# Performance work log

Hardware: AMD Instinct MI355X
Metric: run time of the kernel (lower is better)

Reference implementation:

```python
import jax, jax.numpy as jnp
import numpy as np

B, S, D = 2, 2048, 1024
NH, HD = 16, 64
MLP = 4096
EPS = 1e-6  # flax nnx.RMSNorm default epsilon


def rms_norm(x, scale):
    var = jnp.mean(jnp.square(x.astype(jnp.float32)), axis=-1, keepdims=True)
    return (x * jax.lax.rsqrt(var + EPS)).astype(x.dtype) * scale


def setup_inputs() -> dict:
    key = jax.random.key(0)
    ks = jax.random.split(key, 16)
    lin = lambda k, fin, fout: jax.random.normal(k, (fin, fout), jnp.float32) / np.sqrt(fin)
    x = jax.random.normal(ks[0], (B, S, D), jnp.float32)
    # causal mask [b, s, s]
    mask = jnp.broadcast_to(jnp.tril(jnp.ones((S, S), jnp.bool_))[None], (B, S, S))
    return {
        "x": x,
        "mask": mask,
        "attn_norm_scale": jnp.ones((D,), jnp.float32),
        "q_w": lin(ks[1], D, D), "q_b": jnp.zeros((D,), jnp.float32),
        "k_w": lin(ks[2], D, D), "k_b": jnp.zeros((D,), jnp.float32),
        "v_w": lin(ks[3], D, D), "v_b": jnp.zeros((D,), jnp.float32),
        "o_w": lin(ks[4], D, D), "o_b": jnp.zeros((D,), jnp.float32),
        "ffn_norm_scale": jnp.ones((D,), jnp.float32),
        "gate_w": lin(ks[5], D, MLP), "gate_b": jnp.zeros((MLP,), jnp.float32),
        "up_w": lin(ks[6], D, MLP), "up_b": jnp.zeros((MLP,), jnp.float32),
        "down_w": lin(ks[7], MLP, D), "down_b": jnp.zeros((D,), jnp.float32),
    }


def reference(x, mask, attn_norm_scale, q_w, q_b, k_w, k_b, v_w, v_b, o_w, o_b,
              ffn_norm_scale, gate_w, gate_b, up_w, up_b, down_w, down_b):
    b, s, d = x.shape
    h = rms_norm(x, attn_norm_scale)
    q = (h @ q_w + q_b).reshape(b, s, NH, HD)
    k = (h @ k_w + k_b).reshape(b, s, NH, HD)
    v = (h @ v_w + v_b).reshape(b, s, NH, HD)
    scale = jnp.float32(HD) ** -0.5
    logits = jnp.einsum('bsnh,btnh->bnst', q, k) * scale  # [b, n, s, s]
    logits = jnp.where(mask[:, None, :, :], logits, jnp.finfo(logits.dtype).min)
    attn = jax.nn.softmax(logits.astype(jnp.float32), axis=-1).astype(x.dtype)
    attn_out = jnp.einsum('bnst,btnh->bsnh', attn, v).reshape(b, s, d)
    x = x + attn_out @ o_w + o_b
    h = rms_norm(x, ffn_norm_scale)
    ffn = (jax.nn.silu(h @ gate_w + gate_b) * (h @ up_w + up_b)) @ down_w + down_b
    return x + ffn
```

## Files before the change

kernel.cpp:

```cpp
#include <hip/hip_runtime.h>

#define S_LEN 2048
#define DMODEL 1024
#define NHEADS 16
#define MLPDIM 4096

typedef float f32x4 __attribute__((ext_vector_type(4)));
typedef __bf16 bf16x8 __attribute__((ext_vector_type(8)));
typedef __bf16 bf16x4 __attribute__((ext_vector_type(4)));

__device__ __forceinline__ void gload_lds16(const void* gsrc, void* ldst) {
  __builtin_amdgcn_global_load_lds(
      (const __attribute__((address_space(1))) void*)gsrc,
      (__attribute__((address_space(3))) void*)ldst, 16, 0, 0);
}

#define BARR() __builtin_amdgcn_s_barrier()
#define VMC(n) do { asm volatile("s_waitcnt vmcnt(" #n ")" ::: "memory"); __builtin_amdgcn_sched_barrier(0); } while (0)

__global__ __launch_bounds__(256) void prep_k(
    const float* __restrict__ qw, const float* __restrict__ kw,
    const float* __restrict__ vw, const float* __restrict__ ow,
    const float* __restrict__ gw, const float* __restrict__ uw,
    const float* __restrict__ dw, __bf16* __restrict__ wqkv,
    __bf16* __restrict__ wo, __bf16* __restrict__ wg, __bf16* __restrict__ wu,
    __bf16* __restrict__ wd, const float* __restrict__ qb,
    const float* __restrict__ kb, const float* __restrict__ vb,
    float* __restrict__ bqkv, const float* __restrict__ x,
    const float* __restrict__ ascale, __bf16* __restrict__ hbuf) {
  __shared__ __bf16 tile[64][66];
  __shared__ float part[4];
  int bid = blockIdx.x, t = threadIdx.x;
  if (bid >= 8192) {
    int i = (bid - 8192) * 256 + t;
    if (i < 1024) bqkv[i] = qb[i];
    else if (i < 2048) bqkv[i] = kb[i - 1024];
    else if (i < 3072) bqkv[i] = vb[i - 2048];
    return;
  }
  if (bid >= 4096) {
    int row = bid - 4096;
    f32x4 v = ((const f32x4*)(x + (size_t)row * DMODEL))[t];
    float ss = v[0] * v[0] + v[1] * v[1] + v[2] * v[2] + v[3] * v[3];
#pragma unroll
    for (int off = 1; off < 64; off <<= 1) ss += __shfl_xor(ss, off, 64);
    if ((t & 63) == 0) part[t >> 6] = ss;
    __syncthreads();
    float tot = part[0] + part[1] + part[2] + part[3];
    float r = rsqrtf(tot * (1.0f / DMODEL) + 1e-6f);
    f32x4 s4 = ((const f32x4*)ascale)[t];
    bf16x4 o;
#pragma unroll
    for (int e = 0; e < 4; ++e) o[e] = (__bf16)(v[e] * r * s4[e]);
    ((bf16x4*)hbuf)[(size_t)row * (DMODEL / 4) + t] = o;
    return;
  }
  const float* in;
  __bf16* out;
  int K, N, bx, by;
  if (bid < 1024) {
    int job = bid >> 8, tt = bid & 255;
    K = 1024; N = 1024; bx = tt & 15; by = tt >> 4;
    in = (job == 0) ? qw : (job == 1) ? kw : (job == 2) ? vw : ow;
    out = (job == 0) ? wqkv : (job == 1) ? wqkv + 1024 * 1024
        : (job == 2) ? wqkv + 2 * 1024 * 1024 : wo;
  } else if (bid < 3072) {
    int job = (bid - 1024) >> 10, tt = (bid - 1024) & 1023;
    K = 1024; N = 4096; bx = tt & 63; by = tt >> 6;
    in = job ? uw : gw;
    out = job ? wu : wg;
  } else {
    int tt = bid - 3072;
    K = 4096; N = 1024; bx = tt & 15; by = tt >> 4;
    in = dw; out = wd;
  }
  int n0 = bx * 64, k0 = by * 64;
  int rr = (t & 63) >> 4, sl = t & 15, wv = t >> 6;
#pragma unroll
  for (int j = 0; j < 4; ++j) {
    int r = wv * 4 + rr + j * 16;
    f32x4 v = *(const f32x4*)(in + (size_t)(k0 + r) * N + n0 + sl * 4);
#pragma unroll
    for (int e = 0; e < 4; ++e) tile[r][sl * 4 + e] = (__bf16)v[e];
  }
  __syncthreads();
#pragma unroll
  for (int j = 0; j < 2; ++j) {
    int u = t + j * 256;
    int n = u >> 3, kc = u & 7;
    bf16x8 o;
#pragma unroll
    for (int e = 0; e < 8; ++e) o[e] = tile[kc * 8 + e][n];
    *(bf16x8*)(out + (size_t)(n0 + n) * K + k0 + kc * 8) = o;
  }
}

__global__ __launch_bounds__(256) void rmsnorm_k(
    const float* __restrict__ x, const float* __restrict__ scale,
    __bf16* __restrict__ out) {
  int row = blockIdx.x, tid = threadIdx.x;
  f32x4 v = ((const f32x4*)(x + (size_t)row * DMODEL))[tid];
  float ss = v[0] * v[0] + v[1] * v[1] + v[2] * v[2] + v[3] * v[3];
#pragma unroll
  for (int off = 1; off < 64; off <<= 1) ss += __shfl_xor(ss, off, 64);
  __shared__ float part[4];
  if ((tid & 63) == 0) part[tid >> 6] = ss;
  __syncthreads();
  float tot = part[0] + part[1] + part[2] + part[3];
  float r = rsqrtf(tot * (1.0f / DMODEL) + 1e-6f);
  f32x4 s4 = ((const f32x4*)scale)[tid];
  bf16x4 o;
#pragma unroll
  for (int e = 0; e < 4; ++e) o[e] = (__bf16)(v[e] * r * s4[e]);
  ((bf16x4*)out)[(size_t)row * (DMODEL / 4) + tid] = o;
}

__global__ __launch_bounds__(256, 3) void gemm_qkv(
    const __bf16* __restrict__ A, const __bf16* __restrict__ Bt,
    const float* __restrict__ bias, __bf16* __restrict__ C,
    __bf16* __restrict__ vt, int M, int N, int K) {
  __shared__ __attribute__((aligned(16))) __bf16 As[128 * 64];
  __shared__ __attribute__((aligned(16))) __bf16 Bs[128 * 64];
  int tid = threadIdx.x, lane = tid & 63, wave = tid >> 6;
  int l15 = lane & 15, g4 = lane >> 4;
  int NB = N >> 7, P = M >> 10;
  int xcd = blockIdx.x & 7, j = blockIdx.x >> 3;
  int grp = j / (2 * NB), jj = j - grp * 2 * NB;
  int bm = (xcd * P + grp * 2 + (jj & 1)) * 128;
  int bn = (jj >> 1) * 128;
  int wr = wave >> 1, wc = wave & 1;
  f32x4 acc[4][4] = {};
  const __bf16* Abase = A + (size_t)bm * K;
  const __bf16* Bbase = Bt + (size_t)bn * K;

  for (int k0 = 0; k0 < K; k0 += 64) {
#pragma unroll
    for (int i = 0; i < 4; ++i) {
      int u = tid + i * 256;
      int r = u >> 3, c = (u & 7) ^ (r & 7);
      gload_lds16(Abase + (size_t)r * K + k0 + c * 8, As + u * 8);
      gload_lds16(Bbase + (size_t)r * K + k0 + c * 8, Bs + u * 8);
    }
    __syncthreads();
#pragma unroll
    for (int ks = 0; ks < 2; ++ks) {
      bf16x8 af[4], bfr[4];
#pragma unroll
      for (int m = 0; m < 4; ++m) {
        int r = wr * 64 + m * 16 + l15;
        af[m] = *(const bf16x8*)(As + r * 64 + (((4 * ks + g4) ^ (r & 7)) << 3));
      }
#pragma unroll
      for (int n = 0; n < 4; ++n) {
        int r = wc * 64 + n * 16 + l15;
        bfr[n] = *(const bf16x8*)(Bs + r * 64 + (((4 * ks + g4) ^ (r & 7)) << 3));
      }
      __builtin_amdgcn_s_setprio(1);
#pragma unroll
      for (int m = 0; m < 4; ++m)
#pragma unroll
        for (int n = 0; n < 4; ++n)
          acc[m][n] = __builtin_amdgcn_mfma_f32_16x16x32_bf16(af[m], bfr[n], acc[m][n], 0, 0, 0);
      __builtin_amdgcn_s_setprio(0);
    }
    __syncthreads();
  }
  int r0 = bm + wr * 64 + g4 * 4;
  int c0 = bn + wc * 64 + l15;
  bool isV = (bn >= 2048);
#pragma unroll
  for (int n = 0; n < 4; ++n) {
    int c = c0 + n * 16;
    float bv = bias[c];
#pragma unroll
    for (int m = 0; m < 4; ++m) {
      int rb = r0 + m * 16;
      if (!isV) {
#pragma unroll
        for (int rg = 0; rg < 4; ++rg)
          C[(size_t)(rb + rg) * N + c] = (__bf16)(acc[m][n][rg] + bv);
      } else {
        bf16x4 vv;
#pragma unroll
        for (int rg = 0; rg < 4; ++rg) vv[rg] = (__bf16)(acc[m][n][rg] + bv);
        int b = rb >> 11, s = rb & 2047;
        int sp = (s & ~31) | (((s >> 2) & 3) << 3) | (((s >> 4) & 1) << 2);
        *(bf16x4*)(vt + (size_t)(b * 1024 + c - 2048) * S_LEN + sp) = vv;
      }
    }
  }
}

__global__ __launch_bounds__(256, 4) void gemm_gu(
    const __bf16* __restrict__ A, const __bf16* __restrict__ Gt,
    const __bf16* __restrict__ Ut, const float* __restrict__ gb,
    const float* __restrict__ ub, __bf16* __restrict__ Cout,
    int M, int N, int K) {
  __shared__ __attribute__((aligned(16))) __bf16 As[128 * 64];
  __shared__ __attribute__((aligned(16))) __bf16 Gs[64 * 64];
  __shared__ __attribute__((aligned(16))) __bf16 Us[64 * 64];
  int tid = threadIdx.x, lane = tid & 63, wave = tid >> 6;
  int l15 = lane & 15, g4 = lane >> 4;
  int lin = blockIdx.x;
  int xcd = lin & 7, idx = lin >> 3;
  int bxl = idx >> 4, byl = idx & 15;
  int bn = ((xcd & 3) * 16 + bxl) * 64;
  int bm = ((xcd >> 2) * 16 + byl) * 128;
  int wr = wave >> 1, wc = wave & 1;
  f32x4 ag[4][2] = {}, au[4][2] = {};
  const __bf16* Abase = A + (size_t)bm * K;
  const __bf16* Gbase = Gt + (size_t)bn * K;
  const __bf16* Ubase = Ut + (size_t)bn * K;

  for (int k0 = 0; k0 < K; k0 += 64) {
#pragma unroll
    for (int j = 0; j < 4; ++j) {
      int u = tid + j * 256;
      int r = u >> 3, c = (u & 7) ^ (r & 7);
      gload_lds16(Abase + (size_t)r * K + k0 + c * 8, As + u * 8);
    }
#pragma unroll
    for (int j = 0; j < 2; ++j) {
      int u = tid + j * 256;
      int r = u >> 3, c = (u & 7) ^ (r & 7);
      gload_lds16(Gbase + (size_t)r * K + k0 + c * 8, Gs + u * 8);
      gload_lds16(Ubase + (size_t)r * K + k0 + c * 8, Us + u * 8);
    }
    __syncthreads();
#pragma unroll
    for (int ks = 0; ks < 2; ++ks) {
      bf16x8 af[4], gf[2], uf[2];
#pragma unroll
      for (int m = 0; m < 4; ++m) {
        int r = wr * 64 + m * 16 + l15;
        af[m] = *(const bf16x8*)(As + r * 64 + (((4 * ks + g4) ^ (r & 7)) << 3));
      }
#pragma unroll
      for (int n = 0; n < 2; ++n) {
        int r = wc * 32 + n * 16 + l15;
        int off = r * 64 + (((4 * ks + g4) ^ (r & 7)) << 3);
        gf[n] = *(const bf16x8*)(Gs + off);
        uf[n] = *(const bf16x8*)(Us + off);
      }
      __builtin_amdgcn_s_setprio(1);
#pragma unroll
      for (int m = 0; m < 4; ++m)
#pragma unroll
        for (int n = 0; n < 2; ++n) {
          ag[m][n] = __builtin_amdgcn_mfma_f32_16x16x32_bf16(af[m], gf[n], ag[m][n], 0, 0, 0);
          au[m][n] = __builtin_amdgcn_mfma_f32_16x16x32_bf16(af[m], uf[n], au[m][n], 0, 0, 0);
        }
      __builtin_amdgcn_s_setprio(0);
    }
    __syncthreads();
  }
  int r0 = bm + wr * 64 + g4 * 4;
  int c0 = bn + wc * 32 + l15;
#pragma unroll
  for (int n = 0; n < 2; ++n) {
    int c = c0 + n * 16;
    float gbv = gb[c], ubv = ub[c];
#pragma unroll
    for (int m = 0; m < 4; ++m) {
      int rb = r0 + m * 16;
#pragma unroll
      for (int rg = 0; rg < 4; ++rg) {
        float g = ag[m][n][rg] + gbv;
        float u = au[m][n][rg] + ubv;
        float v = g / (1.0f + __expf(-g)) * u;
        Cout[(size_t)(rb + rg) * N + c] = (__bf16)v;
      }
    }
  }
}

template <int OUT_BF16, int RESID, int SILU>
__global__ __launch_bounds__(256, 3) void gemm_n64(
    const __bf16* __restrict__ A, const __bf16* __restrict__ Bt,
    const float* __restrict__ bias, const float* __restrict__ resid,
    const __bf16* __restrict__ aux, void* __restrict__ Cout,
    int M, int N, int K) {
  __shared__ __attribute__((aligned(16))) __bf16 As[2][128 * 64];
  __shared__ __attribute__((aligned(16))) __bf16 Bs[2][64 * 64];
  int tid = threadIdx.x, lane = tid & 63, wave = tid >> 6;
  int l15 = lane & 15, g4 = lane >> 4;
  int NB = N >> 6;
  int xcd = blockIdx.x & 7, j = blockIdx.x >> 3;
  int grp = j / (2 * NB), jj = j - grp * 2 * NB;
  int bm = (xcd * (M >> 10) + grp * 2 + (jj & 1)) * 128;
  int bn = (jj >> 1) * 64;
  int wr = wave >> 1, wc = wave & 1;
  f32x4 acc[4][2] = {};
  const __bf16* Abase = A + (size_t)bm * K;
  const __bf16* Bbase = Bt + (size_t)bn * K;

  auto stage = [&](int k0, int sb) {
#pragma unroll
    for (int i = 0; i < 4; ++i) {
      int u = tid + i * 256;
      int r = u >> 3, c = (u & 7) ^ (r & 7);
      gload_lds16(Abase + (size_t)r * K + k0 + c * 8, As[sb] + u * 8);
    }
#pragma unroll
    for (int i = 0; i < 2; ++i) {
      int u = tid + i * 256;
      int r = u >> 3, c = (u & 7) ^ (r & 7);
      gload_lds16(Bbase + (size_t)r * K + k0 + c * 8, Bs[sb] + u * 8);
    }
  };

  int NT = K >> 6;
  stage(0, 0);
  for (int t = 0; t < NT; ++t) {
    int sb = t & 1;
    if (t + 1 < NT) { stage((t + 1) << 6, sb ^ 1); VMC(6); }
    else { VMC(0); }
    BARR();
#pragma unroll
    for (int ks = 0; ks < 2; ++ks) {
      bf16x8 af[4], bfr[2];
#pragma unroll
      for (int m = 0; m < 4; ++m) {
        int r = wr * 64 + m * 16 + l15;
        af[m] = *(const bf16x8*)(As[sb] + r * 64 + (((4 * ks + g4) ^ (r & 7)) << 3));
      }
#pragma unroll
      for (int n = 0; n < 2; ++n) {
        int r = wc * 32 + n * 16 + l15;
        bfr[n] = *(const bf16x8*)(Bs[sb] + r * 64 + (((4 * ks + g4) ^ (r & 7)) << 3));
      }
      __builtin_amdgcn_s_setprio(1);
#pragma unroll
      for (int m = 0; m < 4; ++m)
#pragma unroll
        for (int n = 0; n < 2; ++n)
          acc[m][n] = __builtin_amdgcn_mfma_f32_16x16x32_bf16(af[m], bfr[n], acc[m][n], 0, 0, 0);
      __builtin_amdgcn_s_setprio(0);
    }
    BARR();
  }
  int r0 = bm + wr * 64 + g4 * 4;
  int c0 = bn + wc * 32 + l15;
#pragma unroll
  for (int n = 0; n < 2; ++n) {
    int c = c0 + n * 16;
    float bv = bias[c];
#pragma unroll
    for (int m = 0; m < 4; ++m) {
      int rb = r0 + m * 16;
#pragma unroll
      for (int rg = 0; rg < 4; ++rg) {
        int r = rb + rg;
        size_t idx = (size_t)r * N + c;
        float v = acc[m][n][rg] + bv;
        if (SILU) {
          float gg = (float)aux[idx];
          v *= gg / (1.0f + __expf(-gg));
        }
        if (RESID) v += resid[idx];
        if (OUT_BF16) ((__bf16*)Cout)[idx] = (__bf16)v;
        else ((float*)Cout)[idx] = v;
      }
    }
  }
}

#define SCL2E 0.180336879f
__global__ __launch_bounds__(512, 4) void attn_k(
    const __bf16* __restrict__ qkv, const __bf16* __restrict__ vt,
    __bf16* __restrict__ ao) {
  __shared__ __attribute__((aligned(16))) __bf16 Ks[2][128 * 64];
  __shared__ __attribute__((aligned(16))) __bf16 Vs[2][64 * 128];
  int tid = threadIdx.x, lane = tid & 63, w = tid >> 6;
  int l15 = lane & 15, g4 = lane >> 4;
  int bh = blockIdx.x, b = bh >> 4, h = bh & 15;
  int qt = 15 - blockIdx.y;
  int qb = qt * 128;
  int qw = qb + w * 16;
  const __bf16* qkvb = qkv + (size_t)b * S_LEN * 3072 + h * 64;
  const __bf16* kgb = qkvb + 1024;
  const __bf16* vtb = vt + (size_t)b * 1024 * S_LEN + (size_t)(h * 64) * S_LEN;

  bf16x8 qf[2];
#pragma unroll
  for (int ks = 0; ks < 2; ++ks)
    qf[ks] = *(const bf16x8*)(qkvb + (size_t)(qw + l15) * 3072 + 32 * ks + 8 * g4);

  f32x4 oa[4] = {};
  float mrow = -1e30f, lrow = 0.f;
  int q = qw + l15;
  int nt = qt + 1;

  auto stage = [&](int kvb, int buf) {
#pragma unroll
    for (int i = 0; i < 2; ++i) {
      int u = tid + i * 512;
      int r = u >> 3, c = u & 7;
      gload_lds16(kgb + (size_t)(kvb + r) * 3072 + ((c ^ (r & 7)) << 3),
                  Ks[buf] + w * 512 + i * 4096);
    }
#pragma unroll
    for (int i = 0; i < 2; ++i) {
      int u = tid + i * 512;
      int r = u >> 4, cu = u & 15;
      gload_lds16(vtb + (size_t)r * S_LEN + kvb + ((cu ^ (r & 7)) << 3),
                  Vs[buf] + w * 512 + i * 4096);
    }
  };

  stage(0, 0);
  __syncthreads();
  int buf = 0;
  for (int t = 0; t < nt; ++t) {
    int kvb = t * 128;
    if (t + 1 < nt) stage(kvb + 128, buf ^ 1);

    f32x4 sa[8];
#pragma unroll
    for (int i = 0; i < 8; ++i) sa[i] = f32x4{0.f, 0.f, 0.f, 0.f};
#pragma unroll
    for (int st = 0; st < 2; ++st)
#pragma unroll
      for (int ks = 0; ks < 2; ++ks) {
        bf16x8 kf[4];
#pragma unroll
        for (int n = 0; n < 4; ++n) {
          int rr = st * 64 + n * 16 + l15;
          int bc = (64 * ks + 16 * g4) ^ ((rr & 7) << 4);
          kf[n] = *(const bf16x8*)((const char*)Ks[buf] + rr * 128 + bc);
        }
        __builtin_amdgcn_s_setprio(1);
#pragma unroll
        for (int n = 0; n < 4; ++n)
          sa[st * 4 + n] = __builtin_amdgcn_mfma_f32_16x16x32_bf16(kf[n], qf[ks], sa[st * 4 + n], 0, 0, 0);
        __builtin_amdgcn_s_setprio(0);
      }

    bool lastt = (t == nt - 1);
    float nmx = -1e30f;
#pragma unroll
    for (int i = 0; i < 8; ++i)
#pragma unroll
      for (int rg = 0; rg < 4; ++rg) {
        float s = sa[i][rg] * SCL2E;
        if (lastt) {
          int key = kvb + (i >> 2) * 64 + (i & 3) * 16 + 4 * g4 + rg;
          s = (key <= q) ? s : -1e30f;
        }
        sa[i][rg] = s;
        nmx = fmaxf(nmx, s);
      }
    nmx = fmaxf(nmx, __shfl_xor(nmx, 16));
    nmx = fmaxf(nmx, __shfl_xor(nmx, 32));
    float nm;
    if (!__all(nmx <= mrow)) {
      nm = fmaxf(mrow, nmx);
      float sc = exp2f(mrow - nm);
      mrow = nm;
      lrow *= sc;
#pragma unroll
      for (int rg = 0; rg < 4; ++rg) {
        float scq = __shfl(sc, 4 * g4 + rg);
#pragma unroll
        for (int dn = 0; dn < 4; ++dn) oa[dn][rg] *= scq;
      }
    } else {
      nm = mrow;
    }
    float rs = 0.f;
    bf16x8 pa[2][2];
#pragma unroll
    for (int st = 0; st < 2; ++st)
#pragma unroll
      for (int ks = 0; ks < 2; ++ks)
#pragma unroll
        for (int hf = 0; hf < 2; ++hf)
#pragma unroll
          for (int rg = 0; rg < 4; ++rg) {
            float p = exp2f(sa[st * 4 + 2 * ks + hf][rg] - nm);
            rs += p;
            pa[st][ks][hf * 4 + rg] = (__bf16)p;
          }
    rs += __shfl_xor(rs, 16);
    rs += __shfl_xor(rs, 32);
    lrow += rs;

#pragma unroll
    for (int st = 0; st < 2; ++st)
#pragma unroll
      for (int ks = 0; ks < 2; ++ks) {
        __builtin_amdgcn_s_setprio(1);
#pragma unroll
        for (int dn = 0; dn < 4; ++dn) {
          int rr = dn * 16 + l15;
          int swz = (rr & 7) << 4;
          const char* vrow = (const char*)Vs[buf] + rr * 256;
          bf16x8 vf = *(const bf16x8*)(vrow + ((st * 128 + ks * 64 + g4 * 16) ^ swz));
          oa[dn] = __builtin_amdgcn_mfma_f32_16x16x32_bf16(pa[st][ks], vf, oa[dn], 0, 0, 0);
        }
        __builtin_amdgcn_s_setprio(0);
      }
    __syncthreads();
    buf ^= 1;
  }

  __bf16* aobase = ao + (size_t)b * S_LEN * DMODEL + h * 64;
#pragma unroll
  for (int rg = 0; rg < 4; ++rg) {
    float rl = 1.0f / __shfl(lrow, 4 * g4 + rg);
    int qo = qw + 4 * g4 + rg;
#pragma unroll
    for (int dn = 0; dn < 4; ++dn)
      aobase[(size_t)qo * DMODEL + dn * 16 + l15] = (__bf16)(oa[dn][rg] * rl);
  }
}

#define OFF_WQKV 0
#define OFF_WO 6291456
#define OFF_WG 8388608
#define OFF_WU 16777216
#define OFF_WD 25165824
#define OFF_BQKV 33554432
#define OFF_H 33570816
#define OFF_QKV 41959424
#define OFF_AO 67125248
#define OFF_T 75513856
#define OFF_VT OFF_T
#define OFF_X2 109068288

extern "C" void kernel_launch(void* const* d_in, const int* in_sizes, int n_in,
                              void* d_out, int out_size, void* d_ws, size_t ws_size,
                              hipStream_t stream) {
  (void)in_sizes; (void)n_in; (void)out_size; (void)ws_size;
  const float* x = (const float*)d_in[0];
  const float* attn_scale = (const float*)d_in[2];
  const float* q_w = (const float*)d_in[3];
  const float* q_b = (const float*)d_in[4];
  const float* k_w = (const float*)d_in[5];
  const float* k_b = (const float*)d_in[6];
  const float* v_w = (const float*)d_in[7];
  const float* v_b = (const float*)d_in[8];
  const float* o_w = (const float*)d_in[9];
  const float* o_b = (const float*)d_in[10];
  const float* ffn_scale = (const float*)d_in[11];
  const float* gate_w = (const float*)d_in[12];
  const float* gate_b = (const float*)d_in[13];
  const float* up_w = (const float*)d_in[14];
  const float* up_b = (const float*)d_in[15];
  const float* down_w = (const float*)d_in[16];
  const float* down_b = (const float*)d_in[17];

  char* ws = (char*)d_ws;
  __bf16* wqkv = (__bf16*)(ws + OFF_WQKV);
  __bf16* wo = (__bf16*)(ws + OFF_WO);
  __bf16* wg = (__bf16*)(ws + OFF_WG);
  __bf16* wu = (__bf16*)(ws + OFF_WU);
  __bf16* wd = (__bf16*)(ws + OFF_WD);
  float* bqkv = (float*)(ws + OFF_BQKV);
  __bf16* hbuf = (__bf16*)(ws + OFF_H);
  __bf16* qkvbuf = (__bf16*)(ws + OFF_QKV);
  __bf16* aobuf = (__bf16*)(ws + OFF_AO);
  __bf16* tbuf = (__bf16*)(ws + OFF_T);
  __bf16* vtbuf = (__bf16*)(ws + OFF_VT);
  float* x2 = (float*)(ws + OFF_X2);

  dim3 blk(256);
  prep_k<<<dim3(8204), blk, 0, stream>>>(q_w, k_w, v_w, o_w, gate_w, up_w, down_w,
                                         wqkv, wo, wg, wu, wd, q_b, k_b, v_b, bqkv,
                                         x, attn_scale, hbuf);
  gemm_qkv<<<dim3(768), blk, 0, stream>>>(hbuf, wqkv, bqkv, qkvbuf, vtbuf, 4096, 3072, 1024);
  attn_k<<<dim3(32, 16), dim3(512), 0, stream>>>(qkvbuf, vtbuf, aobuf);
  gemm_n64<0, 1, 0><<<dim3(512), blk, 0, stream>>>(aobuf, wo, o_b, x, nullptr, x2, 4096, 1024, 1024);
  rmsnorm_k<<<4096, blk, 0, stream>>>(x2, ffn_scale, hbuf);
  gemm_gu<<<dim3(2048), blk, 0, stream>>>(hbuf, wg, wu, gate_b, up_b, tbuf, 4096, 4096, 1024);
  gemm_n64<0, 1, 0><<<dim3(512), blk, 0, stream>>>(tbuf, wd, down_b, x2, nullptr, (float*)d_out, 4096, 1024, 4096);
}
```

Before: 240.8 us.

## Process two 16-row query groups per wave in attention, halving block threads

The attention kernel now runs 4 waves of 256 threads instead of 8 waves of 512, and each wave handles 32 query rows as two 16-row groups. Each K and V fragment read from LDS feeds two MFMAs, which halves LDS read traffic per MFMA. Staging loops double their iterations to fill the same 128-row K/V tiles. The cost is double the accumulator and score registers per wave and less wave-level parallelism per block to hide latency; launch bounds move to (256, 2).

```diff
diff --git a/kernel.cpp b/kernel.cpp
--- a/kernel.cpp
+++ b/kernel.cpp
@@ -366,7 +366,7 @@
 }
 
 #define SCL2E 0.180336879f
-__global__ __launch_bounds__(512, 4) void attn_k(
+__global__ __launch_bounds__(256, 2) void attn_k(
     const __bf16* __restrict__ qkv, const __bf16* __restrict__ vt,
     __bf16* __restrict__ ao) {
   __shared__ __attribute__((aligned(16))) __bf16 Ks[2][128 * 64];
@@ -376,35 +376,36 @@
   int bh = blockIdx.x, b = bh >> 4, h = bh & 15;
   int qt = 15 - blockIdx.y;
   int qb = qt * 128;
-  int qw = qb + w * 16;
+  int qw = qb + w * 32;
   const __bf16* qkvb = qkv + (size_t)b * S_LEN * 3072 + h * 64;
   const __bf16* kgb = qkvb + 1024;
   const __bf16* vtb = vt + (size_t)b * 1024 * S_LEN + (size_t)(h * 64) * S_LEN;
 
-  bf16x8 qf[2];
-#pragma unroll
-  for (int ks = 0; ks < 2; ++ks)
-    qf[ks] = *(const bf16x8*)(qkvb + (size_t)(qw + l15) * 3072 + 32 * ks + 8 * g4);
-
-  f32x4 oa[4] = {};
-  float mrow = -1e30f, lrow = 0.f;
-  int q = qw + l15;
+  bf16x8 qf[2][2];
+#pragma unroll
+  for (int qg = 0; qg < 2; ++qg)
+#pragma unroll
+    for (int ks = 0; ks < 2; ++ks)
+      qf[qg][ks] = *(const bf16x8*)(qkvb + (size_t)(qw + qg * 16 + l15) * 3072 + 32 * ks + 8 * g4);
+
+  f32x4 oa[2][4] = {};
+  float mrow[2] = {-1e30f, -1e30f}, lrow[2] = {0.f, 0.f};
   int nt = qt + 1;
 
   auto stage = [&](int kvb, int buf) {
 #pragma unroll
-    for (int i = 0; i < 2; ++i) {
-      int u = tid + i * 512;
+    for (int i = 0; i < 4; ++i) {
+      int u = tid + i * 256;
       int r = u >> 3, c = u & 7;
       gload_lds16(kgb + (size_t)(kvb + r) * 3072 + ((c ^ (r & 7)) << 3),
-                  Ks[buf] + w * 512 + i * 4096);
-    }
-#pragma unroll
-    for (int i = 0; i < 2; ++i) {
-      int u = tid + i * 512;
+                  Ks[buf] + w * 512 + i * 2048);
+    }
+#pragma unroll
+    for (int i = 0; i < 4; ++i) {
+      int u = tid + i * 256;
       int r = u >> 4, cu = u & 15;
       gload_lds16(vtb + (size_t)r * S_LEN + kvb + ((cu ^ (r & 7)) << 3),
-                  Vs[buf] + w * 512 + i * 4096);
+                  Vs[buf] + w * 512 + i * 2048);
     }
   };
 
@@ -415,9 +416,11 @@
     int kvb = t * 128;
     if (t + 1 < nt) stage(kvb + 128, buf ^ 1);
 
-    f32x4 sa[8];
-#pragma unroll
-    for (int i = 0; i < 8; ++i) sa[i] = f32x4{0.f, 0.f, 0.f, 0.f};
+    f32x4 sa[2][8];
+#pragma unroll
+    for (int qg = 0; qg < 2; ++qg)
+#pragma unroll
+      for (int i = 0; i < 8; ++i) sa[qg][i] = f32x4{0.f, 0.f, 0.f, 0.f};
 #pragma unroll
     for (int st = 0; st < 2; ++st)
 #pragma unroll
@@ -431,59 +434,65 @@
         }
         __builtin_amdgcn_s_setprio(1);
 #pragma unroll
-        for (int n = 0; n < 4; ++n)
-          sa[st * 4 + n] = __builtin_amdgcn_mfma_f32_16x16x32_bf16(kf[n], qf[ks], sa[st * 4 + n], 0, 0, 0);
+        for (int n = 0; n < 4; ++n) {
+          sa[0][st * 4 + n] = __builtin_amdgcn_mfma_f32_16x16x32_bf16(kf[n], qf[0][ks], sa[0][st * 4 + n], 0, 0, 0);
+          sa[1][st * 4 + n] = __builtin_amdgcn_mfma_f32_16x16x32_bf16(kf[n], qf[1][ks], sa[1][st * 4 + n], 0, 0, 0);
+        }
         __builtin_amdgcn_s_setprio(0);
       }
 
     bool lastt = (t == nt - 1);
-    float nmx = -1e30f;
-#pragma unroll
-    for (int i = 0; i < 8; ++i)
-#pragma unroll
-      for (int rg = 0; rg < 4; ++rg) {
-        float s = sa[i][rg] * SCL2E;
-        if (lastt) {
-          int key = kvb + (i >> 2) * 64 + (i & 3) * 16 + 4 * g4 + rg;
-          s = (key <= q) ? s : -1e30f;
-        }
-        sa[i][rg] = s;
-        nmx = fmaxf(nmx, s);
-      }
-    nmx = fmaxf(nmx, __shfl_xor(nmx, 16));
-    nmx = fmaxf(nmx, __shfl_xor(nmx, 32));
-    float nm;
-    if (!__all(nmx <= mrow)) {
-      nm = fmaxf(mrow, nmx);
-      float sc = exp2f(mrow - nm);
-      mrow = nm;
-      lrow *= sc;
-#pragma unroll
-      for (int rg = 0; rg < 4; ++rg) {
-        float scq = __shfl(sc, 4 * g4 + rg);
-#pragma unroll
-        for (int dn = 0; dn < 4; ++dn) oa[dn][rg] *= scq;
-      }
-    } else {
-      nm = mrow;
-    }
-    float rs = 0.f;
-    bf16x8 pa[2][2];
-#pragma unroll
-    for (int st = 0; st < 2; ++st)
-#pragma unroll
-      for (int ks = 0; ks < 2; ++ks)
-#pragma unroll
-        for (int hf = 0; hf < 2; ++hf)
-#pragma unroll
-          for (int rg = 0; rg < 4; ++rg) {
-            float p = exp2f(sa[st * 4 + 2 * ks + hf][rg] - nm);
-            rs += p;
-            pa[st][ks][hf * 4 + rg] = (__bf16)p;
+    bf16x8 pa[2][2][2];
+#pragma unroll
+    for (int qg = 0; qg < 2; ++qg) {
+      int q = qw + qg * 16 + l15;
+      float nmx = -1e30f;
+#pragma unroll
+      for (int i = 0; i < 8; ++i)
+#pragma unroll
+        for (int rg = 0; rg < 4; ++rg) {
+          float s = sa[qg][i][rg] * SCL2E;
+          if (lastt) {
+            int key = kvb + (i >> 2) * 64 + (i & 3) * 16 + 4 * g4 + rg;
+            s = (key <= q) ? s : -1e30f;
           }
-    rs += __shfl_xor(rs, 16);
-    rs += __shfl_xor(rs, 32);
-    lrow += rs;
+          sa[qg][i][rg] = s;
+          nmx = fmaxf(nmx, s);
+        }
+      nmx = fmaxf(nmx, __shfl_xor(nmx, 16));
+      nmx = fmaxf(nmx, __shfl_xor(nmx, 32));
+      float nm;
+      if (!__all(nmx <= mrow[qg])) {
+        nm = fmaxf(mrow[qg], nmx);
+        float sc = exp2f(mrow[qg] - nm);
+        mrow[qg] = nm;
+        lrow[qg] *= sc;
+#pragma unroll
+        for (int rg = 0; rg < 4; ++rg) {
+          float scq = __shfl(sc, 4 * g4 + rg);
+#pragma unroll
+          for (int dn = 0; dn < 4; ++dn) oa[qg][dn][rg] *= scq;
+        }
+      } else {
+        nm = mrow[qg];
+      }
+      float rs = 0.f;
+#pragma unroll
+      for (int st = 0; st < 2; ++st)
+#pragma unroll
+        for (int ks = 0; ks < 2; ++ks)
+#pragma unroll
+          for (int hf = 0; hf < 2; ++hf)
+#pragma unroll
+            for (int rg = 0; rg < 4; ++rg) {
+              float p = exp2f(sa[qg][st * 4 + 2 * ks + hf][rg] - nm);
+              rs += p;
+              pa[qg][st][ks][hf * 4 + rg] = (__bf16)p;
+            }
+      rs += __shfl_xor(rs, 16);
+      rs += __shfl_xor(rs, 32);
+      lrow[qg] += rs;
+    }
 
 #pragma unroll
     for (int st = 0; st < 2; ++st)
@@ -496,7 +505,8 @@
           int swz = (rr & 7) << 4;
           const char* vrow = (const char*)Vs[buf] + rr * 256;
           bf16x8 vf = *(const bf16x8*)(vrow + ((st * 128 + ks * 64 + g4 * 16) ^ swz));
-          oa[dn] = __builtin_amdgcn_mfma_f32_16x16x32_bf16(pa[st][ks], vf, oa[dn], 0, 0, 0);
+          oa[0][dn] = __builtin_amdgcn_mfma_f32_16x16x32_bf16(pa[0][st][ks], vf, oa[0][dn], 0, 0, 0);
+          oa[1][dn] = __builtin_amdgcn_mfma_f32_16x16x32_bf16(pa[1][st][ks], vf, oa[1][dn], 0, 0, 0);
         }
         __builtin_amdgcn_s_setprio(0);
       }
@@ -506,13 +516,15 @@
 
   __bf16* aobase = ao + (size_t)b * S_LEN * DMODEL + h * 64;
 #pragma unroll
-  for (int rg = 0; rg < 4; ++rg) {
-    float rl = 1.0f / __shfl(lrow, 4 * g4 + rg);
-    int qo = qw + 4 * g4 + rg;
-#pragma unroll
-    for (int dn = 0; dn < 4; ++dn)
-      aobase[(size_t)qo * DMODEL + dn * 16 + l15] = (__bf16)(oa[dn][rg] * rl);
-  }
+  for (int qg = 0; qg < 2; ++qg)
+#pragma unroll
+    for (int rg = 0; rg < 4; ++rg) {
+      float rl = 1.0f / __shfl(lrow[qg], 4 * g4 + rg);
+      int qo = qw + qg * 16 + 4 * g4 + rg;
+#pragma unroll
+      for (int dn = 0; dn < 4; ++dn)
+        aobase[(size_t)qo * DMODEL + dn * 16 + l15] = (__bf16)(oa[qg][dn][rg] * rl);
+    }
 }
 
 #define OFF_WQKV 0
@@ -569,7 +581,7 @@
                                          wqkv, wo, wg, wu, wd, q_b, k_b, v_b, bqkv,
                                          x, attn_scale, hbuf);
   gemm_qkv<<<dim3(768), blk, 0, stream>>>(hbuf, wqkv, bqkv, qkvbuf, vtbuf, 4096, 3072, 1024);
-  attn_k<<<dim3(32, 16), dim3(512), 0, stream>>>(qkvbuf, vtbuf, aobuf);
+  attn_k<<<dim3(32, 16), blk, 0, stream>>>(qkvbuf, vtbuf, aobuf);
   gemm_n64<0, 1, 0><<<dim3(512), blk, 0, stream>>>(aobuf, wo, o_b, x, nullptr, x2, 4096, 1024, 1024);
   rmsnorm_k<<<4096, blk, 0, stream>>>(x2, ffn_scale, hbuf);
   gemm_gu<<<dim3(2048), blk, 0, stream>>>(hbuf, wg, wu, gate_b, up_b, tbuf, 4096, 4096, 1024);
```

Result: slower. 254.6 us (+5.7%).

## Enlarge gate/up GEMM tiles to 256x128 with double-buffered LDS pipeline

Applied to the files above, without the earlier changes.

Replaces the gate/up fused GEMM with an 8-wave, 512-thread kernel that computes 256x128 output tiles, giving more data reuse per LDS load. It also double-buffers LDS and splits each k-step into four phases that interleave the next tile's global-to-LDS loads with MFMA work, using vmcnt and lgkmcnt waits. LDS use grows to 128KB per block and more accumulators are held in registers. This cuts the block count to 512 and may lower occupancy.

```diff
diff --git a/kernel.cpp b/kernel.cpp
--- a/kernel.cpp
+++ b/kernel.cpp
@@ -16,6 +16,7 @@
 }
 
 #define BARR() __builtin_amdgcn_s_barrier()
+#define LGKM0() do { asm volatile("s_waitcnt lgkmcnt(0)" ::: "memory"); __builtin_amdgcn_sched_barrier(0); } while (0)
 #define VMC(n) do { asm volatile("s_waitcnt vmcnt(" #n ")" ::: "memory"); __builtin_amdgcn_sched_barrier(0); } while (0)
 
 __global__ __launch_bounds__(256) void prep_k(
@@ -191,82 +192,110 @@
   }
 }
 
-__global__ __launch_bounds__(256, 4) void gemm_gu(
+__global__ __launch_bounds__(512, 2) void gemm_gu8(
     const __bf16* __restrict__ A, const __bf16* __restrict__ Gt,
     const __bf16* __restrict__ Ut, const float* __restrict__ gb,
     const float* __restrict__ ub, __bf16* __restrict__ Cout,
     int M, int N, int K) {
-  __shared__ __attribute__((aligned(16))) __bf16 As[128 * 64];
-  __shared__ __attribute__((aligned(16))) __bf16 Gs[64 * 64];
-  __shared__ __attribute__((aligned(16))) __bf16 Us[64 * 64];
+  __shared__ __attribute__((aligned(16))) __bf16 As[2][256 * 64];
+  __shared__ __attribute__((aligned(16))) __bf16 Gs[2][128 * 64];
+  __shared__ __attribute__((aligned(16))) __bf16 Us[2][128 * 64];
   int tid = threadIdx.x, lane = tid & 63, wave = tid >> 6;
   int l15 = lane & 15, g4 = lane >> 4;
-  int lin = blockIdx.x;
-  int xcd = lin & 7, idx = lin >> 3;
-  int bxl = idx >> 4, byl = idx & 15;
-  int bn = ((xcd & 3) * 16 + bxl) * 64;
-  int bm = ((xcd >> 2) * 16 + byl) * 128;
-  int wr = wave >> 1, wc = wave & 1;
-  f32x4 ag[4][2] = {}, au[4][2] = {};
+  int xcd = blockIdx.x & 7, idx = blockIdx.x >> 3;
+  int byl = idx & 7, bxl = idx >> 3;
+  int bn = ((xcd & 3) * 8 + bxl) * 128;
+  int bm = ((xcd >> 2) * 8 + byl) * 256;
+  int wr = wave >> 2, wc = wave & 3;
+  f32x4 ag[8][2] = {}, au[8][2] = {};
   const __bf16* Abase = A + (size_t)bm * K;
   const __bf16* Gbase = Gt + (size_t)bn * K;
   const __bf16* Ubase = Ut + (size_t)bn * K;
 
-  for (int k0 = 0; k0 < K; k0 += 64) {
-#pragma unroll
-    for (int j = 0; j < 4; ++j) {
-      int u = tid + j * 256;
-      int r = u >> 3, c = (u & 7) ^ (r & 7);
-      gload_lds16(Abase + (size_t)r * K + k0 + c * 8, As + u * 8);
-    }
-#pragma unroll
-    for (int j = 0; j < 2; ++j) {
-      int u = tid + j * 256;
-      int r = u >> 3, c = (u & 7) ^ (r & 7);
-      gload_lds16(Gbase + (size_t)r * K + k0 + c * 8, Gs + u * 8);
-      gload_lds16(Ubase + (size_t)r * K + k0 + c * 8, Us + u * 8);
-    }
-    __syncthreads();
-#pragma unroll
-    for (int ks = 0; ks < 2; ++ks) {
-      bf16x8 af[4], gf[2], uf[2];
+  int r0s = tid >> 3;
+  int cs = (tid & 7) ^ (r0s & 7);
+  size_t K2 = (size_t)K;
+
+  auto stageA = [&](int h, int kt, int sb) {
+    const __bf16* g0 = Abase + (size_t)(h * 128 + r0s) * K2 + kt * 64 + cs * 8;
+    gload_lds16(g0, &As[sb][h * 8192] + tid * 8);
+    gload_lds16(g0 + (size_t)64 * K2, &As[sb][h * 8192 + 4096] + tid * 8);
+  };
+  auto stageG = [&](int kt, int sb) {
+    const __bf16* g0 = Gbase + (size_t)r0s * K2 + kt * 64 + cs * 8;
+    gload_lds16(g0, &Gs[sb][0] + tid * 8);
+    gload_lds16(g0 + (size_t)64 * K2, &Gs[sb][4096] + tid * 8);
+  };
+  auto stageU = [&](int kt, int sb) {
+    const __bf16* g0 = Ubase + (size_t)r0s * K2 + kt * 64 + cs * 8;
+    gload_lds16(g0, &Us[sb][0] + tid * 8);
+    gload_lds16(g0 + (size_t)64 * K2, &Us[sb][4096] + tid * 8);
+  };
+
+  int NT = K >> 6;
+  stageA(0, 0, 0);
+  stageG(0, 0);
+  stageU(0, 0);
+  stageA(1, 0, 0);
+  VMC(0);
+  BARR();
+
+  bf16x8 gf[2], uf[2];
+  for (int t = 0; t < NT; ++t) {
+    int sb = t & 1;
+#pragma unroll
+    for (int p = 0; p < 4; ++p) {
+      int mh = p & 1, ks = p >> 1;
+      if (t + 1 < NT) {
+        if (p == 0) stageA(0, t + 1, sb ^ 1);
+        else if (p == 1) stageG(t + 1, sb ^ 1);
+        else if (p == 2) stageU(t + 1, sb ^ 1);
+        else stageA(1, t + 1, sb ^ 1);
+      }
+      if (p <= 1) { VMC(4); }
+      BARR();
+      bf16x8 af[4];
 #pragma unroll
       for (int m = 0; m < 4; ++m) {
-        int r = wr * 64 + m * 16 + l15;
-        af[m] = *(const bf16x8*)(As + r * 64 + (((4 * ks + g4) ^ (r & 7)) << 3));
-      }
-#pragma unroll
-      for (int n = 0; n < 2; ++n) {
-        int r = wc * 32 + n * 16 + l15;
-        int off = r * 64 + (((4 * ks + g4) ^ (r & 7)) << 3);
-        gf[n] = *(const bf16x8*)(Gs + off);
-        uf[n] = *(const bf16x8*)(Us + off);
-      }
+        int r = wr * 128 + mh * 64 + m * 16 + l15;
+        af[m] = *(const bf16x8*)(&As[sb][0] + r * 64 + (((4 * ks + g4) ^ (r & 7)) << 3));
+      }
+      if (mh == 0) {
+#pragma unroll
+        for (int n = 0; n < 2; ++n) {
+          int r = wc * 32 + n * 16 + l15;
+          int off = r * 64 + (((4 * ks + g4) ^ (r & 7)) << 3);
+          gf[n] = *(const bf16x8*)(&Gs[sb][0] + off);
+          uf[n] = *(const bf16x8*)(&Us[sb][0] + off);
+        }
+      }
+      LGKM0();
       __builtin_amdgcn_s_setprio(1);
 #pragma unroll
       for (int m = 0; m < 4; ++m)
 #pragma unroll
         for (int n = 0; n < 2; ++n) {
-          ag[m][n] = __builtin_amdgcn_mfma_f32_16x16x32_bf16(af[m], gf[n], ag[m][n], 0, 0, 0);
-          au[m][n] = __builtin_amdgcn_mfma_f32_16x16x32_bf16(af[m], uf[n], au[m][n], 0, 0, 0);
+          ag[mh * 4 + m][n] = __builtin_amdgcn_mfma_f32_16x16x32_bf16(af[m], gf[n], ag[mh * 4 + m][n], 0, 0, 0);
+          au[mh * 4 + m][n] = __builtin_amdgcn_mfma_f32_16x16x32_bf16(af[m], uf[n], au[mh * 4 + m][n], 0, 0, 0);
         }
       __builtin_amdgcn_s_setprio(0);
-    }
-    __syncthreads();
-  }
-  int r0 = bm + wr * 64 + g4 * 4;
+      if (p == 3) BARR();
+    }
+  }
+
+  int r0 = bm + wr * 128 + g4 * 4;
   int c0 = bn + wc * 32 + l15;
 #pragma unroll
   for (int n = 0; n < 2; ++n) {
     int c = c0 + n * 16;
     float gbv = gb[c], ubv = ub[c];
 #pragma unroll
-    for (int m = 0; m < 4; ++m) {
-      int rb = r0 + m * 16;
+    for (int am = 0; am < 8; ++am) {
+      int rb = r0 + (am >> 2) * 64 + (am & 3) * 16;
 #pragma unroll
       for (int rg = 0; rg < 4; ++rg) {
-        float g = ag[m][n][rg] + gbv;
-        float u = au[m][n][rg] + ubv;
+        float g = ag[am][n][rg] + gbv;
+        float u = au[am][n][rg] + ubv;
         float v = g / (1.0f + __expf(-g)) * u;
         Cout[(size_t)(rb + rg) * N + c] = (__bf16)v;
       }
@@ -572,6 +601,6 @@
   attn_k<<<dim3(32, 16), dim3(512), 0, stream>>>(qkvbuf, vtbuf, aobuf);
   gemm_n64<0, 1, 0><<<dim3(512), blk, 0, stream>>>(aobuf, wo, o_b, x, nullptr, x2, 4096, 1024, 1024);
   rmsnorm_k<<<4096, blk, 0, stream>>>(x2, ffn_scale, hbuf);
-  gemm_gu<<<dim3(2048), blk, 0, stream>>>(hbuf, wg, wu, gate_b, up_b, tbuf, 4096, 4096, 1024);
+  gemm_gu8<<<dim3(512), dim3(512), 0, stream>>>(hbuf, wg, wu, gate_b, up_b, tbuf, 4096, 4096, 1024);
   gemm_n64<0, 1, 0><<<dim3(512), blk, 0, stream>>>(tbuf, wd, down_b, x2, nullptr, (float*)d_out, 4096, 1024, 4096);
 }
```

Result: slower. 255.0 us (+5.9%).
